# Optimization experiments

Hardware: AMD Instinct MI355X
Metric: run time of the kernel (lower is better)

## Reference

```python
import jax, jax.numpy as jnp
import numpy as np

N, NNODES, CIN, COUT = 64, 512, 32, 64


def setup_inputs() -> dict:
    key = jax.random.key(0)
    k1, k2, k3, k4, k5 = jax.random.split(key, 5)
    A = jax.random.normal(k1, (N, NNODES, NNODES), dtype=jnp.float32)
    X = jax.random.normal(k2, (N, NNODES, CIN), dtype=jnp.float32)
    A_coeffs = jax.random.normal(k3, (5 + 2 * CIN,), dtype=jnp.float32)
    x_num = 4 + 2 * CIN
    scale = np.sqrt(2.0) / (COUT + x_num)
    X_coeffs_1 = jax.random.normal(k4, (COUT, x_num), dtype=jnp.float32) * scale
    X_coeffs_2 = jax.random.normal(k5, (COUT, x_num), dtype=jnp.float32) * scale
    return {"A": A, "X": X, "A_coeffs": A_coeffs,
            "X_coeffs_1": X_coeffs_1, "X_coeffs_2": X_coeffs_2}


def _forward(A, X, A_coeffs, W1, W2):
    n = A.shape[-1]
    C = X.shape[-1]
    Xt = jnp.swapaxes(X, -1, -2)                      # N,C,n
    diag = jnp.diagonal(A, axis1=-2, axis2=-1)        # N,n
    mean_diag = diag.mean(-1)                         # N
    mean_cols = A.mean(-1)                            # N,n
    mean_all = mean_cols.mean(-1)                     # N
    mean_X = Xt.mean(-1)                              # N,C

    c = A_coeffs
    w6 = c[5:5 + C]                                   # coeffs for a6 (X_i + X_j)
    w7 = c[5 + C:5 + 2 * C]                           # coeffs for a7 (mean_X)
    # Fold the 'd,ndij->nij' contraction over the 7 basis tensors into
    # scalar/row/col broadcast terms (identical math, no N x (5+2C) x n x n tensor).
    s = jnp.einsum('c,nci->ni', w6, Xt)               # N,n
    const = c[1] * mean_all + c[2] * mean_diag + jnp.einsum('c,nc->n', w7, mean_X)
    vec = c[3] * mean_cols + c[4] * diag + s          # N,n
    A_t = c[0] * A + const[:, None, None] + vec[:, :, None] + vec[:, None, :]

    # X basis out_x: N x (4+2C) x n, order [x1, x2, x3, x4, x5, x6]
    ones_n = jnp.ones((1, 1, n), A.dtype)
    out_x = jnp.concatenate([
        Xt,                                           # x1: N,C,n
        mean_X[:, :, None] * ones_n,                  # x2: N,C,n
        mean_cols[:, None, :],                        # x3: N,1,n
        diag[:, None, :],                             # x4: N,1,n
        mean_diag[:, None, None] * ones_n,            # x5: N,1,n
        mean_all[:, None, None] * ones_n,             # x6: N,1,n
    ], axis=1)
    X1 = jnp.einsum('bd,ndi->nbi', W1, out_x)         # N,B,n
    X2 = jnp.einsum('bd,ndi->nbi', W2, out_x)         # N,B,n
    out = jnp.einsum('nij,nbj->nbi', A_t, X1) / n + X2  # N,B,n
    return jnp.swapaxes(out, -1, -2)                  # N,n,B


def reference(A, X, A_coeffs, X_coeffs_1, X_coeffs_2):
    return _forward(A, X, A_coeffs, X_coeffs_1, X_coeffs_2)
```

## Files before the change

kernel.cpp:

```cpp
#include <hip/hip_runtime.h>
#include <hip/hip_bf16.h>

#define NB 64
#define NN 512
#define CI 32
#define CO 64
#define XN 68

typedef __attribute__((ext_vector_type(8))) short bf16x8;
typedef __attribute__((ext_vector_type(4))) float f32x4;

__device__ inline short f2bf(float f) {
  union { __hip_bfloat16 h; unsigned short u; } cv;
  cv.h = __float2bfloat16(f);
  return (short)cv.u;
}

__device__ inline bf16x8 cvt8(float4 a, float4 b) {
  bf16x8 r;
  r[0] = f2bf(a.x); r[1] = f2bf(a.y); r[2] = f2bf(a.z); r[3] = f2bf(a.w);
  r[4] = f2bf(b.x); r[5] = f2bf(b.y); r[6] = f2bf(b.z); r[7] = f2bf(b.w);
  return r;
}

__device__ __forceinline__ void gld16(const void* g, void* l) {
  __builtin_amdgcn_global_load_lds(
      (const __attribute__((address_space(1))) unsigned int*)g,
      (__attribute__((address_space(3))) unsigned int*)l, 16, 0, 0);
}

__global__ __launch_bounds__(256) void k1x(
    const float* __restrict__ A, const float* __restrict__ X,
    const float* __restrict__ cf, const float* __restrict__ W1,
    float* __restrict__ mc, float* __restrict__ dg, float* __restrict__ vec,
    float* __restrict__ pA, float* __restrict__ pD,
    float* __restrict__ pmX, float* __restrict__ ptC, float* __restrict__ pS,
    unsigned short* __restrict__ Ybf, unsigned short* __restrict__ Abf) {
  int b = blockIdx.x, ch = blockIdx.y;
  int t = threadIdx.x, w = t >> 6, lane = t & 63;
  int r0 = ch * 16;
  int kb = r0 >> 5, jbase = r0 & 16;
  const float* Ab = A + (size_t)b * NN * NN;
  __shared__ float sXc[16][33];
  __shared__ float scf[69];
  __shared__ float sMc[16], sDg[16], sVec[16], wsum[4];

  if (t < 69) scf[t] = cf[t];
  {
    int j = t >> 4, c = (t & 15) * 2;
    float2 xv = *(const float2*)(X + ((size_t)b * NN + r0 + j) * CI + c);
    sXc[j][c] = xv.x; sXc[j][c + 1] = xv.y;
  }
  float4 v0[4], v1[4];
#pragma unroll
  for (int m = 0; m < 4; ++m) {
    const float* rp = Ab + (size_t)(r0 + w * 4 + m) * NN;
    v0[m] = *(const float4*)(rp + lane * 4);
    v1[m] = *(const float4*)(rp + 256 + lane * 4);
  }
  float accR = 0.f;
#pragma unroll
  for (int m = 0; m < 4; ++m) {
    float s = (v0[m].x + v0[m].y) + (v0[m].z + v0[m].w) +
              (v1[m].x + v1[m].y) + (v1[m].z + v1[m].w);
#pragma unroll
    for (int off = 1; off < 64; off <<= 1) s += __shfl_xor(s, off, 64);
    if (lane == 0) {
      float m_ = s * (1.0f / NN);
      mc[b * NN + r0 + w * 4 + m] = m_;
      sMc[w * 4 + m] = m_;
    }
    accR += s;
  }
  if (lane == 0) wsum[w] = accR;
  if (t < 16) {
    float d = Ab[(size_t)(r0 + t) * NN + r0 + t];
    dg[b * NN + r0 + t] = d;
    sDg[t] = d;
  }

  {
    int ic5 = ch >> 2;
    int lrb = (ch & 3) * 16 + w * 4;
    size_t bb = ((size_t)(b * 8 + ic5)) * 8 * 4096;
    int c5a = lane >> 4;
    int Ka = (lane & 15) >> 1;
    int sub = (lane & 1) << 2;
#pragma unroll
    for (int m = 0; m < 4; ++m) {
      int lr = lrb + m;
      int sl = ((Ka ^ (lr & 7)) << 3) + sub;
      union { unsigned short u[4]; uint2 v; } p0, p1;
      p0.u[0] = (unsigned short)f2bf(v0[m].x); p0.u[1] = (unsigned short)f2bf(v0[m].y);
      p0.u[2] = (unsigned short)f2bf(v0[m].z); p0.u[3] = (unsigned short)f2bf(v0[m].w);
      p1.u[0] = (unsigned short)f2bf(v1[m].x); p1.u[1] = (unsigned short)f2bf(v1[m].y);
      p1.u[2] = (unsigned short)f2bf(v1[m].z); p1.u[3] = (unsigned short)f2bf(v1[m].w);
      *(uint2*)(Abf + bb + (size_t)c5a * 4096 + lr * 64 + sl) = p0.v;
      *(uint2*)(Abf + bb + (size_t)(4 + c5a) * 4096 + lr * 64 + sl) = p1.v;
    }
  }
  __syncthreads();

  float c0n = scf[0] * (1.0f / NN);

  if (t < 16) {
    float u = 0.f;
#pragma unroll
    for (int c = 0; c < CI; ++c) u += scf[5 + c] * sXc[t][c];
    float vj = scf[3] * sMc[t] + scf[4] * sDg[t] + u;
    vec[b * NN + r0 + t] = vj;
    sVec[t] = vj;
  } else if (t == 16) {
    pA[b * 32 + ch] = wsum[0] + wsum[1] + wsum[2] + wsum[3];
    float sd = 0.f;
#pragma unroll
    for (int k = 0; k < 16; ++k) sd += sDg[k];
    pD[b * 32 + ch] = sd;
  }

  {
    int ra = lane & 15, kg = lane >> 4, g = lane >> 4;
    const float* wp = W1 + (w * 16 + ra) * XN + kg * 8;
    bf16x8 wf = cvt8(*(const float4*)wp, *(const float4*)(wp + 4));
    const float* xp = &sXc[ra][kg * 8];
    bf16x8 xf = cvt8(*(const float4*)xp, *(const float4*)(xp + 4));
    f32x4 zero = {0.f, 0.f, 0.f, 0.f};
    f32x4 d = __builtin_amdgcn_mfma_f32_16x16x32_bf16(xf, wf, zero, 0, 0, 0);
    union { unsigned short u[4]; uint2 v; } pk;
#pragma unroll
    for (int r = 0; r < 4; ++r) pk.u[r] = (unsigned short)f2bf(d[r] * c0n);
    int o = w * 16 + ra;
    *(uint2*)(Ybf + (((size_t)b * 16 + kb) * 80 + o) * 32 + jbase + g * 4) = pk.v;
  }
  if (t < 16) {
    Ybf[(((size_t)b * 16 + kb) * 80 + 64) * 32 + jbase + t] =
        (unsigned short)f2bf(sMc[t] * c0n);
  } else if (t < 32) {
    Ybf[(((size_t)b * 16 + kb) * 80 + 65) * 32 + jbase + (t - 16)] =
        (unsigned short)f2bf(sDg[t - 16] * c0n);
  } else if (t < 32 + 224) {
    int u2 = t - 32;
    int row = 66 + (u2 >> 4), col = jbase + (u2 & 15);
    Ybf[(((size_t)b * 16 + kb) * 80 + row) * 32 + col] = 0;
  }
  __syncthreads();

  if (t < 32) {
    float s1 = 0.f, s2 = 0.f;
#pragma unroll
    for (int r = 0; r < 16; ++r) {
      float xv = sXc[r][t];
      s1 += xv;
      s2 += sVec[r] * xv;
    }
    pmX[((size_t)b * 32 + ch) * 32 + t] = s1;
    ptC[((size_t)b * 32 + ch) * 32 + t] = s2;
  } else if (t < 35) {
    float s = 0.f;
    if (t == 32) { for (int r = 0; r < 16; ++r) s += sVec[r]; }
    if (t == 33) { for (int r = 0; r < 16; ++r) s += sVec[r] * sMc[r]; }
    if (t == 34) { for (int r = 0; r < 16; ++r) s += sVec[r] * sDg[r]; }
    pS[((size_t)b * 32 + ch) * 3 + (t - 32)] = s;
  }
}

__global__ __launch_bounds__(256) void kW(
    const float* __restrict__ cf, const float* __restrict__ W1,
    const float* __restrict__ W2, const float* __restrict__ pA,
    const float* __restrict__ pD, const float* __restrict__ pmX,
    const float* __restrict__ ptC, const float* __restrict__ pS,
    float* __restrict__ colv, float* __restrict__ sconst) {
  int gb = blockIdx.x, t = threadIdx.x;
  int bb0 = gb * 4;
  __shared__ float sW1[64][69], sW2[64][69];
  __shared__ float mXs[4][33], tCs[4][33];
  __shared__ float scal[4][6];
  __shared__ float scf[69];
  if (t < 69) scf[t] = cf[t];
  for (int idx = t; idx < 64 * XN; idx += 256) {
    int r = idx / XN, c = idx - r * XN;
    sW1[r][c] = W1[idx];
    sW2[r][c] = W2[idx];
  }
  if (t < 128) {
    int bb = t >> 5, c = t & 31, b = bb0 + bb;
    float s1 = 0.f, s2 = 0.f;
#pragma unroll
    for (int k = 0; k < 32; ++k) {
      s1 += pmX[((size_t)b * 32 + k) * 32 + c];
      s2 += ptC[((size_t)b * 32 + k) * 32 + c];
    }
    mXs[bb][c] = s1 * (1.0f / NN);
    tCs[bb][c] = s2;
  } else if (t < 132) {
    int bb = t - 128, b = bb0 + bb;
    float sA = 0.f, sD = 0.f;
#pragma unroll
    for (int k = 0; k < 32; ++k) { sA += pA[b * 32 + k]; sD += pD[b * 32 + k]; }
    scal[bb][0] = sD * (1.0f / NN);
    scal[bb][1] = sA * (1.0f / ((float)NN * (float)NN));
  } else if (t < 136) {
    int bb = t - 132, b = bb0 + bb;
    float s1 = 0.f, s2 = 0.f, s3 = 0.f;
#pragma unroll
    for (int k = 0; k < 32; ++k) {
      s1 += pS[((size_t)b * 32 + k) * 3 + 0];
      s2 += pS[((size_t)b * 32 + k) * 3 + 1];
      s3 += pS[((size_t)b * 32 + k) * 3 + 2];
    }
    scal[bb][2] = s1; scal[bb][3] = s2; scal[bb][4] = s3;
  }
  __syncthreads();
  if (t < 4) {
    float s7 = 0.f;
#pragma unroll
    for (int c = 0; c < CI; ++c) s7 += scf[5 + CI + c] * mXs[t][c];
    sconst[bb0 + t] = scf[1] * scal[t][1] + scf[2] * scal[t][0] + s7;
  }
  {
    int bb = t >> 6, o = t & 63, b = bb0 + bb;
    float w1mX = 0.f, a1 = 0.f, a2 = 0.f, wt = 0.f;
#pragma unroll
    for (int c = 0; c < CI; ++c) {
      float m = mXs[bb][c];
      w1mX += sW1[o][c] * m;
      a1 += sW1[o][CI + c] * m;
      a2 += sW2[o][CI + c] * m;
      wt += sW1[o][c] * tCs[bb][c];
    }
    float smd = scal[bb][0], sma = scal[bb][1];
    a1 += sW1[o][66] * smd + sW1[o][67] * sma;
    a2 += sW2[o][66] * smd + sW2[o][67] * sma;
    float we0 = sW1[o][64], we1 = sW1[o][65];
    float S1n = w1mX + a1 + we0 * sma + we1 * smd;
    float SVn = (wt + a1 * scal[bb][2] + we0 * scal[bb][3] + we1 * scal[bb][4]) * (1.0f / NN);
    float4 cva = make_float4(S1n, a2 + SVn, sW2[o][64] + scf[0] * a1, sW2[o][65]);
    float4 cvb = make_float4(we0, we1, 0.f, 0.f);
    *(float4*)&colv[((size_t)b * CO + o) * 8] = cva;
    *(float4*)&colv[((size_t)b * CO + o) * 8 + 4] = cvb;
  }
}

__global__ __launch_bounds__(512, 8) void k5_mfma(
    const unsigned short* __restrict__ Abf, const unsigned short* __restrict__ Ybf,
    const float* __restrict__ X, const float* __restrict__ W2,
    const float* __restrict__ vec, const float* __restrict__ mc,
    const float* __restrict__ dg, const float* __restrict__ colv,
    const float* __restrict__ sconst, float* __restrict__ out) {
  int ic = blockIdx.x, b = blockIdx.y;
  int t = threadIdx.x, w = t >> 6, lane = t & 63;
  int rg = w >> 1, oc = w & 1;
  int ra = lane & 15, kg = lane >> 4, g = lane >> 4;
  int i0 = ic * 64;
  int wr0 = rg * 16;
  __shared__ unsigned short sA[2][4096];
  __shared__ unsigned short sB[2][5120];
  __shared__ float sGm[64], sGd[64];

  const unsigned short* Asrc = Abf + ((size_t)(b * 8 + ic)) * 8 * 4096;
  const unsigned short* Bsrc = Ybf + (size_t)b * 16 * 80 * 32;

  int aoff = w * 512 + lane * 8;
  int boff2 = (8 + w) * 512 + lane * 8;

  {
    gld16(Asrc + aoff, &sA[0][w * 512]);
    gld16(Bsrc + aoff, &sB[0][w * 512]);
    if (w < 2) gld16(Bsrc + boff2, &sB[0][(8 + w) * 512]);
  }
  __syncthreads();

  f32x4 acc[2] = {{0.f, 0.f, 0.f, 0.f}, {0.f, 0.f, 0.f, 0.f}};
  f32x4 acc4 = {0.f, 0.f, 0.f, 0.f};
  int arow = wr0 + ra;
  int abase = arow * 64;
  int aswz = arow & 7;

  for (int c = 0; c < 8; ++c) {
    int cur = c & 1;
    if (c < 7) {
      const unsigned short* an = Asrc + (size_t)(c + 1) * 4096;
      const unsigned short* bn = Bsrc + (size_t)(c + 1) * 5120;
      gld16(an + aoff, &sA[cur ^ 1][w * 512]);
      gld16(bn + aoff, &sB[cur ^ 1][w * 512]);
      if (w < 2) gld16(bn + boff2, &sB[cur ^ 1][(8 + w) * 512]);
    }
#pragma unroll
    for (int kbl = 0; kbl < 2; ++kbl) {
      bf16x8 af = *(const bf16x8*)&sA[cur][abase + (((kbl * 4 + kg) ^ aswz) << 3)];
#pragma unroll
      for (int to = 0; to < 2; ++to) {
        int grow = kbl * 80 + oc * 32 + to * 16 + ra;
        bf16x8 bf = *(const bf16x8*)&sB[cur][grow * 32 + kg * 8];
        acc[to] = __builtin_amdgcn_mfma_f32_16x16x32_bf16(af, bf, acc[to], 0, 0, 0);
      }
      if (oc == 0) {
        bf16x8 bf4 = *(const bf16x8*)&sB[cur][(kbl * 80 + 64 + ra) * 32 + kg * 8];
        acc4 = __builtin_amdgcn_mfma_f32_16x16x32_bf16(af, bf4, acc4, 0, 0, 0);
      }
    }
    __syncthreads();
  }

  {
    const float* xp = X + (size_t)(b * NN + i0 + wr0 + ra) * CI + kg * 8;
    bf16x8 xf = cvt8(*(const float4*)xp, *(const float4*)(xp + 4));
#pragma unroll
    for (int to = 0; to < 2; ++to) {
      const float* wp = W2 + (size_t)(oc * 32 + to * 16 + ra) * XN + kg * 8;
      bf16x8 wf = cvt8(*(const float4*)wp, *(const float4*)(wp + 4));
      acc[to] = __builtin_amdgcn_mfma_f32_16x16x32_bf16(xf, wf, acc[to], 0, 0, 0);
    }
  }

  if (oc == 0 && ra < 2) {
#pragma unroll
    for (int r = 0; r < 4; ++r) {
      if (ra == 0) sGm[wr0 + g * 4 + r] = acc4[r];
      else         sGd[wr0 + g * 4 + r] = acc4[r];
    }
  }
  __syncthreads();

  float4 v4 = *(const float4*)&vec[b * NN + i0 + wr0 + g * 4];
  float4 m4 = *(const float4*)&mc[b * NN + i0 + wr0 + g * 4];
  float4 d4 = *(const float4*)&dg[b * NN + i0 + wr0 + g * 4];
  float sc = sconst[b];
  float vp[4] = {v4.x + sc, v4.y + sc, v4.z + sc, v4.w + sc};
  float mr[4] = {m4.x, m4.y, m4.z, m4.w};
  float dr[4] = {d4.x, d4.y, d4.z, d4.w};
  float Gm[4], Gd[4];
#pragma unroll
  for (int r = 0; r < 4; ++r) {
    int row = wr0 + g * 4 + r;
    Gm[r] = sGm[row];
    Gd[r] = sGd[row];
  }

#pragma unroll
  for (int to = 0; to < 2; ++to) {
    int o = oc * 32 + to * 16 + ra;
    float4 cva = *(const float4*)&colv[((size_t)b * CO + o) * 8];
    float4 cvb = *(const float4*)&colv[((size_t)b * CO + o) * 8 + 4];
#pragma unroll
    for (int r = 0; r < 4; ++r) {
      float val = acc[to][r] + vp[r] * cva.x + cva.y + mr[r] * cva.z +
                  dr[r] * cva.w + Gm[r] * cvb.x + Gd[r] * cvb.y;
      out[((size_t)(b * NN + i0 + wr0 + g * 4 + r)) * CO + o] = val;
    }
  }
}

extern "C" void kernel_launch(void* const* d_in, const int* in_sizes, int n_in,
                              void* d_out, int out_size, void* d_ws, size_t ws_size,
                              hipStream_t stream) {
  const float* A = (const float*)d_in[0];
  const float* X = (const float*)d_in[1];
  const float* cf = (const float*)d_in[2];
  const float* W1 = (const float*)d_in[3];
  const float* W2 = (const float*)d_in[4];
  float* out = (float*)d_out;

  float* p = (float*)d_ws;
  float* mc = p;      p += NB * NN;
  float* dg = p;      p += NB * NN;
  float* vec = p;     p += NB * NN;
  float* pA = p;      p += NB * 32;
  float* pD = p;      p += NB * 32;
  float* pmX = p;     p += NB * 32 * 32;
  float* ptC = p;     p += NB * 32 * 32;
  float* pS = p;      p += NB * 32 * 3;
  float* colv = p;    p += NB * CO * 8;
  float* sconst = p;  p += NB;
  unsigned short* Ybf = (unsigned short*)p;
  unsigned short* Abf = Ybf + (size_t)NB * 16 * 80 * 32;

  k1x<<<dim3(NB, 32), 256, 0, stream>>>(A, X, cf, W1, mc, dg, vec,
                                        pA, pD, pmX, ptC, pS, Ybf, Abf);
  kW<<<16, 256, 0, stream>>>(cf, W1, W2, pA, pD, pmX, ptC, pS, colv, sconst);
  k5_mfma<<<dim3(8, NB), 512, 0, stream>>>(Abf, Ybf, X, W2, vec, mc, dg,
                                           colv, sconst, out);
}
```

Before: 45.99 us.

## Split K across wave pairs with direct global loads and LDS reduction in MFMA kernel

The k5 MFMA kernel drops its double-buffered LDS staging of A and Y tiles. Each wave now loads bf16 fragments straight from global memory and covers all 64 output columns for half of the K dimension. The two K-halves are then summed through a small shared buffer, and the diag/mean G terms move from LDS to lane shuffles. This removes the per-chunk syncs and the LDS copies, at the cost of more global/L2 traffic (B is re-read per wave), less latency hiding, and half the waves idling in the epilogue.

```diff
diff --git a/kernel.cpp b/kernel.cpp
--- a/kernel.cpp
+++ b/kernel.cpp
@@ -21,12 +21,6 @@
   r[0] = f2bf(a.x); r[1] = f2bf(a.y); r[2] = f2bf(a.z); r[3] = f2bf(a.w);
   r[4] = f2bf(b.x); r[5] = f2bf(b.y); r[6] = f2bf(b.z); r[7] = f2bf(b.w);
   return r;
-}
-
-__device__ __forceinline__ void gld16(const void* g, void* l) {
-  __builtin_amdgcn_global_load_lds(
-      (const __attribute__((address_space(1))) unsigned int*)g,
-      (__attribute__((address_space(3))) unsigned int*)l, 16, 0, 0);
 }
 
 __global__ __launch_bounds__(256) void k1x(
@@ -241,7 +235,7 @@
   }
 }
 
-__global__ __launch_bounds__(512, 8) void k5_mfma(
+__global__ __launch_bounds__(512, 4) void k5_mfma(
     const unsigned short* __restrict__ Abf, const unsigned short* __restrict__ Ybf,
     const float* __restrict__ X, const float* __restrict__ W2,
     const float* __restrict__ vec, const float* __restrict__ mc,
@@ -249,104 +243,98 @@
     const float* __restrict__ sconst, float* __restrict__ out) {
   int ic = blockIdx.x, b = blockIdx.y;
   int t = threadIdx.x, w = t >> 6, lane = t & 63;
-  int rg = w >> 1, oc = w & 1;
+  int rg = w >> 1, kh = w & 1;
   int ra = lane & 15, kg = lane >> 4, g = lane >> 4;
-  int i0 = ic * 64;
-  int wr0 = rg * 16;
-  __shared__ unsigned short sA[2][4096];
-  __shared__ unsigned short sB[2][5120];
-  __shared__ float sGm[64], sGd[64];
+  int i0 = ic * 64, wr0 = rg * 16;
+  __shared__ float sAcc[4][16][64];
+  __shared__ float sG4[4][16][2];
 
   const unsigned short* Asrc = Abf + ((size_t)(b * 8 + ic)) * 8 * 4096;
   const unsigned short* Bsrc = Ybf + (size_t)b * 16 * 80 * 32;
 
-  int aoff = w * 512 + lane * 8;
-  int boff2 = (8 + w) * 512 + lane * 8;
-
-  {
-    gld16(Asrc + aoff, &sA[0][w * 512]);
-    gld16(Bsrc + aoff, &sB[0][w * 512]);
-    if (w < 2) gld16(Bsrc + boff2, &sB[0][(8 + w) * 512]);
+  int arow = wr0 + ra, abase = arow * 64, aswz = arow & 7;
+
+  f32x4 acc[4] = {{0.f, 0.f, 0.f, 0.f}, {0.f, 0.f, 0.f, 0.f},
+                  {0.f, 0.f, 0.f, 0.f}, {0.f, 0.f, 0.f, 0.f}};
+  f32x4 acc4 = {0.f, 0.f, 0.f, 0.f};
+
+#pragma unroll
+  for (int jt = 0; jt < 8; ++jt) {
+    int jj = kh * 8 + jt;
+    int c = jj >> 1, kbl = jj & 1;
+    bf16x8 af = *(const bf16x8*)&Asrc[(size_t)c * 4096 + abase +
+                                      (((kbl * 4 + kg) ^ aswz) << 3)];
+    const unsigned short* Bb = Bsrc + (size_t)jj * 80 * 32;
+#pragma unroll
+    for (int to = 0; to < 4; ++to) {
+      bf16x8 bf = *(const bf16x8*)&Bb[(to * 16 + ra) * 32 + kg * 8];
+      acc[to] = __builtin_amdgcn_mfma_f32_16x16x32_bf16(af, bf, acc[to], 0, 0, 0);
+    }
+    bf16x8 bf4 = *(const bf16x8*)&Bb[(64 + ra) * 32 + kg * 8];
+    acc4 = __builtin_amdgcn_mfma_f32_16x16x32_bf16(af, bf4, acc4, 0, 0, 0);
+  }
+
+  if (kh == 1) {
+#pragma unroll
+    for (int to = 0; to < 4; ++to)
+#pragma unroll
+      for (int r = 0; r < 4; ++r)
+        sAcc[rg][g * 4 + r][to * 16 + ra] = acc[to][r];
+    if (ra < 2) {
+#pragma unroll
+      for (int r = 0; r < 4; ++r) sG4[rg][g * 4 + r][ra] = acc4[r];
+    }
   }
   __syncthreads();
 
-  f32x4 acc[2] = {{0.f, 0.f, 0.f, 0.f}, {0.f, 0.f, 0.f, 0.f}};
-  f32x4 acc4 = {0.f, 0.f, 0.f, 0.f};
-  int arow = wr0 + ra;
-  int abase = arow * 64;
-  int aswz = arow & 7;
-
-  for (int c = 0; c < 8; ++c) {
-    int cur = c & 1;
-    if (c < 7) {
-      const unsigned short* an = Asrc + (size_t)(c + 1) * 4096;
-      const unsigned short* bn = Bsrc + (size_t)(c + 1) * 5120;
-      gld16(an + aoff, &sA[cur ^ 1][w * 512]);
-      gld16(bn + aoff, &sB[cur ^ 1][w * 512]);
-      if (w < 2) gld16(bn + boff2, &sB[cur ^ 1][(8 + w) * 512]);
-    }
-#pragma unroll
-    for (int kbl = 0; kbl < 2; ++kbl) {
-      bf16x8 af = *(const bf16x8*)&sA[cur][abase + (((kbl * 4 + kg) ^ aswz) << 3)];
-#pragma unroll
-      for (int to = 0; to < 2; ++to) {
-        int grow = kbl * 80 + oc * 32 + to * 16 + ra;
-        bf16x8 bf = *(const bf16x8*)&sB[cur][grow * 32 + kg * 8];
-        acc[to] = __builtin_amdgcn_mfma_f32_16x16x32_bf16(af, bf, acc[to], 0, 0, 0);
+  if (kh == 0) {
+#pragma unroll
+    for (int to = 0; to < 4; ++to)
+#pragma unroll
+      for (int r = 0; r < 4; ++r)
+        acc[to][r] += sAcc[rg][g * 4 + r][to * 16 + ra];
+    if (ra < 2) {
+#pragma unroll
+      for (int r = 0; r < 4; ++r) acc4[r] += sG4[rg][g * 4 + r][ra];
+    }
+
+    {
+      const float* xp = X + (size_t)(b * NN + i0 + wr0 + ra) * CI + kg * 8;
+      bf16x8 xf = cvt8(*(const float4*)xp, *(const float4*)(xp + 4));
+#pragma unroll
+      for (int to = 0; to < 4; ++to) {
+        const float* wp = W2 + (size_t)(to * 16 + ra) * XN + kg * 8;
+        bf16x8 wf = cvt8(*(const float4*)wp, *(const float4*)(wp + 4));
+        acc[to] = __builtin_amdgcn_mfma_f32_16x16x32_bf16(xf, wf, acc[to], 0, 0, 0);
       }
-      if (oc == 0) {
-        bf16x8 bf4 = *(const bf16x8*)&sB[cur][(kbl * 80 + 64 + ra) * 32 + kg * 8];
-        acc4 = __builtin_amdgcn_mfma_f32_16x16x32_bf16(af, bf4, acc4, 0, 0, 0);
+    }
+
+    float Gm[4], Gd[4];
+#pragma unroll
+    for (int r = 0; r < 4; ++r) {
+      Gm[r] = __shfl(acc4[r], lane & 48, 64);
+      Gd[r] = __shfl(acc4[r], (lane & 48) | 1, 64);
+    }
+
+    float4 v4 = *(const float4*)&vec[b * NN + i0 + wr0 + g * 4];
+    float4 m4 = *(const float4*)&mc[b * NN + i0 + wr0 + g * 4];
+    float4 d4 = *(const float4*)&dg[b * NN + i0 + wr0 + g * 4];
+    float sc = sconst[b];
+    float vp[4] = {v4.x + sc, v4.y + sc, v4.z + sc, v4.w + sc};
+    float mr[4] = {m4.x, m4.y, m4.z, m4.w};
+    float dr[4] = {d4.x, d4.y, d4.z, d4.w};
+
+#pragma unroll
+    for (int to = 0; to < 4; ++to) {
+      int o = to * 16 + ra;
+      float4 cva = *(const float4*)&colv[((size_t)b * CO + o) * 8];
+      float4 cvb = *(const float4*)&colv[((size_t)b * CO + o) * 8 + 4];
+#pragma unroll
+      for (int r = 0; r < 4; ++r) {
+        float val = acc[to][r] + vp[r] * cva.x + cva.y + mr[r] * cva.z +
+                    dr[r] * cva.w + Gm[r] * cvb.x + Gd[r] * cvb.y;
+        out[((size_t)(b * NN + i0 + wr0 + g * 4 + r)) * CO + o] = val;
       }
-    }
-    __syncthreads();
-  }
-
-  {
-    const float* xp = X + (size_t)(b * NN + i0 + wr0 + ra) * CI + kg * 8;
-    bf16x8 xf = cvt8(*(const float4*)xp, *(const float4*)(xp + 4));
-#pragma unroll
-    for (int to = 0; to < 2; ++to) {
-      const float* wp = W2 + (size_t)(oc * 32 + to * 16 + ra) * XN + kg * 8;
-      bf16x8 wf = cvt8(*(const float4*)wp, *(const float4*)(wp + 4));
-      acc[to] = __builtin_amdgcn_mfma_f32_16x16x32_bf16(xf, wf, acc[to], 0, 0, 0);
-    }
-  }
-
-  if (oc == 0 && ra < 2) {
-#pragma unroll
-    for (int r = 0; r < 4; ++r) {
-      if (ra == 0) sGm[wr0 + g * 4 + r] = acc4[r];
-      else         sGd[wr0 + g * 4 + r] = acc4[r];
-    }
-  }
-  __syncthreads();
-
-  float4 v4 = *(const float4*)&vec[b * NN + i0 + wr0 + g * 4];
-  float4 m4 = *(const float4*)&mc[b * NN + i0 + wr0 + g * 4];
-  float4 d4 = *(const float4*)&dg[b * NN + i0 + wr0 + g * 4];
-  float sc = sconst[b];
-  float vp[4] = {v4.x + sc, v4.y + sc, v4.z + sc, v4.w + sc};
-  float mr[4] = {m4.x, m4.y, m4.z, m4.w};
-  float dr[4] = {d4.x, d4.y, d4.z, d4.w};
-  float Gm[4], Gd[4];
-#pragma unroll
-  for (int r = 0; r < 4; ++r) {
-    int row = wr0 + g * 4 + r;
-    Gm[r] = sGm[row];
-    Gd[r] = sGd[row];
-  }
-
-#pragma unroll
-  for (int to = 0; to < 2; ++to) {
-    int o = oc * 32 + to * 16 + ra;
-    float4 cva = *(const float4*)&colv[((size_t)b * CO + o) * 8];
-    float4 cvb = *(const float4*)&colv[((size_t)b * CO + o) * 8 + 4];
-#pragma unroll
-    for (int r = 0; r < 4; ++r) {
-      float val = acc[to][r] + vp[r] * cva.x + cva.y + mr[r] * cva.z +
-                  dr[r] * cva.w + Gm[r] * cvb.x + Gd[r] * cvb.y;
-      out[((size_t)(b * NN + i0 + wr0 + g * 4 + r)) * CO + o] = val;
     }
   }
 }
```

New measurement: 47.44 us. 3.1% more time.

## Replace global-to-LDS direct loads with register-staged two-deep prefetch and padded B tile

Applied to the files above, without the earlier changes.

Drops the global_load_lds direct copies and instead loads the next-next A and B chunks into registers, writing them to the other LDS buffer after the MFMA work of the current chunk. The B tile row stride is padded from 32 to 40 shorts to cut LDS bank conflicts on the B fragment reads. Launch bounds drop the minimum occupancy hint from 8 to 2 blocks so the extra staging registers fit. In exchange the kernel uses more registers and LDS, and may run fewer resident waves.

```diff
diff --git a/kernel.cpp b/kernel.cpp
--- a/kernel.cpp
+++ b/kernel.cpp
@@ -21,12 +21,6 @@
   r[0] = f2bf(a.x); r[1] = f2bf(a.y); r[2] = f2bf(a.z); r[3] = f2bf(a.w);
   r[4] = f2bf(b.x); r[5] = f2bf(b.y); r[6] = f2bf(b.z); r[7] = f2bf(b.w);
   return r;
-}
-
-__device__ __forceinline__ void gld16(const void* g, void* l) {
-  __builtin_amdgcn_global_load_lds(
-      (const __attribute__((address_space(1))) unsigned int*)g,
-      (__attribute__((address_space(3))) unsigned int*)l, 16, 0, 0);
 }
 
 __global__ __launch_bounds__(256) void k1x(
@@ -241,7 +235,7 @@
   }
 }
 
-__global__ __launch_bounds__(512, 8) void k5_mfma(
+__global__ __launch_bounds__(512, 2) void k5_mfma(
     const unsigned short* __restrict__ Abf, const unsigned short* __restrict__ Ybf,
     const float* __restrict__ X, const float* __restrict__ W2,
     const float* __restrict__ vec, const float* __restrict__ mc,
@@ -254,20 +248,30 @@
   int i0 = ic * 64;
   int wr0 = rg * 16;
   __shared__ unsigned short sA[2][4096];
-  __shared__ unsigned short sB[2][5120];
+  __shared__ unsigned short sB[2][160 * 40];
   __shared__ float sGm[64], sGd[64];
 
   const unsigned short* Asrc = Abf + ((size_t)(b * 8 + ic)) * 8 * 4096;
-  const unsigned short* Bsrc = Ybf + (size_t)b * 16 * 80 * 32;
-
-  int aoff = w * 512 + lane * 8;
-  int boff2 = (8 + w) * 512 + lane * 8;
-
-  {
-    gld16(Asrc + aoff, &sA[0][w * 512]);
-    gld16(Bsrc + aoff, &sB[0][w * 512]);
-    if (w < 2) gld16(Bsrc + boff2, &sB[0][(8 + w) * 512]);
-  }
+  const unsigned short* Yb = Ybf + (size_t)b * 16 * 80 * 32;
+
+  int b1_row = t >> 2, b1_sub = t & 3;
+  int b2_row = 128 + (t >> 2), b2_sub = t & 3;
+  bool hasb2 = (t < 128);
+
+  {
+    uint4 av = *(const uint4*)(Asrc + t * 8);
+    *(uint4*)&sA[0][t * 8] = av;
+    uint4 v1 = *(const uint4*)(Yb + b1_row * 32 + b1_sub * 8);
+    *(uint4*)&sB[0][b1_row * 40 + b1_sub * 8] = v1;
+    if (hasb2) {
+      uint4 v2 = *(const uint4*)(Yb + b2_row * 32 + b2_sub * 8);
+      *(uint4*)&sB[0][b2_row * 40 + b2_sub * 8] = v2;
+    }
+  }
+  uint4 rCa = *(const uint4*)(Asrc + 4096 + t * 8);
+  uint4 rCb1 = *(const uint4*)(Yb + 160 * 32 + b1_row * 32 + b1_sub * 8);
+  uint4 rCb2;
+  if (hasb2) rCb2 = *(const uint4*)(Yb + 160 * 32 + b2_row * 32 + b2_sub * 8);
   __syncthreads();
 
   f32x4 acc[2] = {{0.f, 0.f, 0.f, 0.f}, {0.f, 0.f, 0.f, 0.f}};
@@ -278,26 +282,34 @@
 
   for (int c = 0; c < 8; ++c) {
     int cur = c & 1;
-    if (c < 7) {
-      const unsigned short* an = Asrc + (size_t)(c + 1) * 4096;
-      const unsigned short* bn = Bsrc + (size_t)(c + 1) * 5120;
-      gld16(an + aoff, &sA[cur ^ 1][w * 512]);
-      gld16(bn + aoff, &sB[cur ^ 1][w * 512]);
-      if (w < 2) gld16(bn + boff2, &sB[cur ^ 1][(8 + w) * 512]);
-    }
+    uint4 rNa, rNb1, rNb2;
+    if (c < 6) {
+      rNa = *(const uint4*)(Asrc + (size_t)(c + 2) * 4096 + t * 8);
+      const unsigned short* nsrc = Yb + (size_t)(c + 2) * 160 * 32;
+      rNb1 = *(const uint4*)(nsrc + b1_row * 32 + b1_sub * 8);
+      if (hasb2) rNb2 = *(const uint4*)(nsrc + b2_row * 32 + b2_sub * 8);
+    }
+    __builtin_amdgcn_sched_barrier(0);
 #pragma unroll
     for (int kbl = 0; kbl < 2; ++kbl) {
       bf16x8 af = *(const bf16x8*)&sA[cur][abase + (((kbl * 4 + kg) ^ aswz) << 3)];
 #pragma unroll
       for (int to = 0; to < 2; ++to) {
         int grow = kbl * 80 + oc * 32 + to * 16 + ra;
-        bf16x8 bf = *(const bf16x8*)&sB[cur][grow * 32 + kg * 8];
+        bf16x8 bf = *(const bf16x8*)&sB[cur][grow * 40 + kg * 8];
         acc[to] = __builtin_amdgcn_mfma_f32_16x16x32_bf16(af, bf, acc[to], 0, 0, 0);
       }
       if (oc == 0) {
-        bf16x8 bf4 = *(const bf16x8*)&sB[cur][(kbl * 80 + 64 + ra) * 32 + kg * 8];
+        bf16x8 bf4 = *(const bf16x8*)&sB[cur][(kbl * 80 + 64 + ra) * 40 + kg * 8];
         acc4 = __builtin_amdgcn_mfma_f32_16x16x32_bf16(af, bf4, acc4, 0, 0, 0);
       }
+    }
+    if (c < 7) {
+      *(uint4*)&sA[cur ^ 1][t * 8] = rCa;
+      *(uint4*)&sB[cur ^ 1][b1_row * 40 + b1_sub * 8] = rCb1;
+      if (hasb2) *(uint4*)&sB[cur ^ 1][b2_row * 40 + b2_sub * 8] = rCb2;
+      rCa = rNa; rCb1 = rNb1;
+      if (hasb2) rCb2 = rNb2;
     }
     __syncthreads();
   }
```

Result: no change. 45.87 us, median of 3 (-0.3%).
